# Performance work log

Hardware: AMD Instinct MI355X
Metric: run time of the kernel (lower is better)

The kernel has to match this reference:

```python
import jax, jax.numpy as jnp
import numpy as np

B, C, N = 2, 32, 4096
EPS = 1e-5


def _batchnorm1d(x, gamma, bias):
    # BatchNorm1d in training mode: stats over (batch, spatial) per channel, biased var
    mean = x.mean(axis=(0, 2), keepdims=True)
    var = x.var(axis=(0, 2), keepdims=True)
    return (x - mean) * jax.lax.rsqrt(var + EPS) * gamma[None, :, None] + bias[None, :, None]


def setup_inputs() -> dict:
    key = jax.random.key(0)
    k1, k2, k3 = jax.random.split(key, 3)
    Feature = jax.random.normal(k1, (B, C, N), dtype=jnp.float32)
    gamma = jnp.ones((C,), dtype=jnp.float32)
    bn_bias = jnp.zeros((C,), dtype=jnp.float32)
    alpha = jax.random.uniform(k2, (), dtype=jnp.float32)
    beta = jax.random.uniform(k3, (), dtype=jnp.float32)
    return {"Feature": Feature, "gamma": gamma, "bn_bias": bn_bias, "alpha": alpha, "beta": beta}


def reference(Feature, gamma, bn_bias, alpha, beta):
    a = Feature                                   # [B, C, N]
    # --- PAM: BN + ReLU prologue, then spatial N x N attention ---
    f = jax.nn.relu(_batchnorm1d(Feature, gamma, bn_bias))
    cb = jnp.einsum('bcn,bcm->bnm', f, f)         # c^T c : [B, N, N]
    s = jax.nn.softmax(cb, axis=1)                # softmax over dim=1 (as in source)
    e_p = jnp.einsum('bcn,bmn->bcm', f, s)        # c @ s^T : [B, C, N]
    pam = alpha * e_p + a
    # --- CAM: channel C x C attention, softmax over batch axis (dim=0 as in source) ---
    aa = jnp.einsum('bcn,bdn->bdc', a, a)         # matmul(a, a^T).permute(0,2,1) : [B, C, C]
    x = jax.nn.softmax(aa, axis=0)
    e_c = jnp.einsum('bji,bjn->bin', x, a)        # x^T @ a : [B, C, N]
    cam = beta * e_c + a
    return pam + cam
```

## Files before the change

### kernel.cpp

```cpp
#include <hip/hip_runtime.h>
#include <math.h>


#define BB 2
#define CC 32
#define NN 4096
#define EPSV 1e-5f

typedef short short8 __attribute__((ext_vector_type(8)));
typedef float f32x4 __attribute__((ext_vector_type(4)));

#define OFF_FNC  0
#define OFF_FCN  131072
#define OFF_M    262144
#define OFF_SC   270336
#define OFF_SH   270368
#define OFF_XW   270400
#define OFF_AAP  272448
#define OFF_Z    305216
#define OFF_EP   313408
#define ZERO_BASE 305216
#define ZERO_N4   67584

__device__ inline ushort f2bf(float x) {
    uint u = __float_as_uint(x);
    uint r = u + 0x7FFFu + ((u >> 16) & 1u);
    return (ushort)(r >> 16);
}
__device__ inline float bf2f(ushort h) { return __uint_as_float(((uint)h) << 16); }
__device__ inline uint packbf(float lo, float hi) {
    return (__float_as_uint(hi) & 0xFFFF0000u) | (__float_as_uint(lo) >> 16);
}

__global__ void __launch_bounds__(256) k_pre(const float* __restrict__ x,
                                             const float* __restrict__ gamma,
                                             const float* __restrict__ bias,
                                             float* __restrict__ ws) {
    __shared__ float smem[4352];
    const int blk = blockIdx.x, t = threadIdx.x;
    const int lane = t & 63, wv = t >> 6;
    if (blk < 32) {
        const int c = blk;
        float s = 0.f, s2 = 0.f;
        for (int i = t; i < BB * NN; i += 256) {
            const int bb = i >> 12, n = i & (NN - 1);
            const float v = x[((size_t)(bb * CC + c)) * NN + n];
            s += v; s2 += v * v;
        }
        for (int off = 32; off; off >>= 1) { s += __shfl_down(s, off); s2 += __shfl_down(s2, off); }
        if (lane == 0) { smem[wv] = s; smem[4 + wv] = s2; }
        __syncthreads();
        if (t == 0) {
            const float S = smem[0] + smem[1] + smem[2] + smem[3];
            const float S2 = smem[4] + smem[5] + smem[6] + smem[7];
            const float mean = S * (1.f / (BB * NN));
            const float var = S2 * (1.f / (BB * NN)) - mean * mean;
            const float sc = gamma[c] * rsqrtf(var + EPSV);
            ws[OFF_SC + c] = sc;
            ws[OFF_SH + c] = bias[c] - mean * sc;
        }
    } else if (blk < 96) {
        const int blk2 = blk - 32;
        const int b = blk2 >> 4, chnk = blk2 & 15;
        const int nb = chnk * 256;
        const int d = t >> 3, cg4 = (t & 7) * 4;
        float a0 = 0.f, a1 = 0.f, a2 = 0.f, a3 = 0.f;
        for (int it = 0; it < 2; ++it) {
            __syncthreads();
            for (int li = t; li < 4096; li += 256) {
                const int row = li >> 7, col = li & 127;
                smem[row * 132 + col] = x[((size_t)(b * CC + row)) * NN + nb + it * 128 + col];
            }
            __syncthreads();
            for (int k = 0; k < 128; ++k) {
                const float vd = smem[d * 132 + k];
                a0 += smem[(cg4 + 0) * 132 + k] * vd;
                a1 += smem[(cg4 + 1) * 132 + k] * vd;
                a2 += smem[(cg4 + 2) * 132 + k] * vd;
                a3 += smem[(cg4 + 3) * 132 + k] * vd;
            }
        }
        float* dst = ws + OFF_AAP + ((size_t)((b * 16 + chnk) * CC + d)) * CC + cg4;
        dst[0] = a0; dst[1] = a1; dst[2] = a2; dst[3] = a3;
    } else {
        for (int gid = (blk - 96) * 256 + t; gid < ZERO_N4; gid += 416 * 256)
            ((float4*)(ws + ZERO_BASE))[gid] = make_float4(0.f, 0.f, 0.f, 0.f);
    }
}

__global__ void __launch_bounds__(256) k_makef(const float* __restrict__ x,
                                               float* __restrict__ ws) {
    const int blk = blockIdx.x, t = threadIdx.x;
    const int ch = t & 31;
    const float sc = ws[OFF_SC + ch], sh = ws[OFF_SH + ch];
    #pragma unroll
    for (int it = 0; it < 2; ++it) {
        const int col = (t >> 5) + it * 8;
        const int idx = blk * 16 + col;
        const int b = idx >> 12, n = idx & (NN - 1);
        const float v = x[((size_t)(b * CC + ch)) * NN + n];
        const float f = fmaxf(v * sc + sh, 0.f);
        const ushort h = f2bf(f);
        const float fr = bf2f(h);
        ((ushort*)(ws + OFF_FNC))[(size_t)idx * CC + ch] = h;
        ((ushort*)(ws + OFF_FCN))[((size_t)(b * CC + ch)) * NN + n] = h;
        float s = fr * fr;
        s += __shfl_xor(s, 1); s += __shfl_xor(s, 2); s += __shfl_xor(s, 4);
        s += __shfl_xor(s, 8); s += __shfl_xor(s, 16);
        if (ch == 0) ws[OFF_M + idx] = s;
    }
    if (blk == 511) {
        for (int li = t; li < CC * CC; li += 256) {
            const int i = li >> 5, j = li & 31;
            float q0 = 0.f, q1 = 0.f;
            for (int cchunk = 0; cchunk < 16; ++cchunk) {
                q0 += ws[OFF_AAP + ((size_t)((0 * 16 + cchunk) * CC + j)) * CC + i];
                q1 += ws[OFF_AAP + ((size_t)((1 * 16 + cchunk) * CC + j)) * CC + i];
            }
            const float mx = fmaxf(q0, q1);
            const float e0 = __expf(q0 - mx), e1 = __expf(q1 - mx);
            const float inv = 1.f / (e0 + e1);
            ws[OFF_XW + 0 * 1024 + i * 32 + j] = e0 * inv;
            ws[OFF_XW + 1 * 1024 + i * 32 + j] = e1 * inv;
        }
    }
}

__global__ void __launch_bounds__(256) k_zpass(float* __restrict__ ws) {
    const ushort* fnc = (const ushort*)(ws + OFF_FNC);
    const int blk = blockIdx.x, t = threadIdx.x;
    const int lane = t & 63, wv = t >> 6;
    const int ml = lane & 15, kg = lane >> 4;
    const f32x4 fzero = {0.f, 0.f, 0.f, 0.f};
    const int b = blk >> 9;
    const int rem = blk & 511;
    const int ng = rem >> 4;
    const int mch = rem & 15;
    const int nbA = ng * 128 + wv * 16, nbB = nbA + 64;
    const short8 bfA = *(const short8*)(fnc + ((size_t)(b * NN + nbA + ml)) * CC + kg * 8);
    const short8 bfB = *(const short8*)(fnc + ((size_t)(b * NN + nbB + ml)) * CC + kg * 8);
    const float MA = ws[OFF_M + b * NN + nbA + ml];
    const float MB = ws[OFF_M + b * NN + nbB + ml];
    float zA = 0.f, zB = 0.f;
    const int m0 = mch * 256;
    for (int mm = m0; mm < m0 + 256; mm += 16) {
        const short8 af = *(const short8*)(fnc + ((size_t)(b * NN + mm + ml)) * CC + kg * 8);
        f32x4 dA = __builtin_amdgcn_mfma_f32_16x16x32_bf16(af, bfA, fzero, 0, 0, 0);
        f32x4 dB = __builtin_amdgcn_mfma_f32_16x16x32_bf16(af, bfB, fzero, 0, 0, 0);
        zA += __expf(dA[0] - MA) + __expf(dA[1] - MA) + __expf(dA[2] - MA) + __expf(dA[3] - MA);
        zB += __expf(dB[0] - MB) + __expf(dB[1] - MB) + __expf(dB[2] - MB) + __expf(dB[3] - MB);
    }
    zA += __shfl_xor(zA, 16); zA += __shfl_xor(zA, 32);
    zB += __shfl_xor(zB, 16); zB += __shfl_xor(zB, 32);
    if (lane < 16) {
        atomicAdd(ws + OFF_Z + b * NN + nbA + ml, zA);
        atomicAdd(ws + OFF_Z + b * NN + nbB + ml, zB);
    }
}

__global__ void __launch_bounds__(256) k_eppass(float* __restrict__ ws) {
    const ushort* fnc = (const ushort*)(ws + OFF_FNC);
    const ushort* fcn = (const ushort*)(ws + OFF_FCN);
    const int blk = blockIdx.x, t = threadIdx.x;
    const int lane = t & 63, wv = t >> 6;
    const int ml = lane & 15, kg = lane >> 4;
    const f32x4 fzero = {0.f, 0.f, 0.f, 0.f};
    const int b = blk >> 9;
    const int rem = blk & 511;
    const int mg = rem >> 3;
    const int nch = rem & 7;
    const int mb = mg * 64 + wv * 16;
    const short8 bm = *(const short8*)(fnc + ((size_t)(b * NN + mb + ml)) * CC + kg * 8);
    f32x4 acc0 = fzero, acc1 = fzero;
    const float* Mp = ws + OFF_M + b * NN;
    const float* Zp = ws + OFF_Z + b * NN;
    const int n0beg = nch * 512;
    for (int n0 = n0beg; n0 < n0beg + 512; n0 += 32) {
        const short8 an0 = *(const short8*)(fnc + ((size_t)(b * NN + n0      + ml)) * CC + kg * 8);
        const short8 an1 = *(const short8*)(fnc + ((size_t)(b * NN + n0 + 16 + ml)) * CC + kg * 8);
        f32x4 d0 = __builtin_amdgcn_mfma_f32_16x16x32_bf16(an0, bm, fzero, 0, 0, 0);
        f32x4 d1 = __builtin_amdgcn_mfma_f32_16x16x32_bf16(an1, bm, fzero, 0, 0, 0);
        const float4 M0 = *(const float4*)(Mp + n0 + kg * 4);
        const float4 M1 = *(const float4*)(Mp + n0 + 16 + kg * 4);
        const float4 Z0 = *(const float4*)(Zp + n0 + kg * 4);
        const float4 Z1 = *(const float4*)(Zp + n0 + 16 + kg * 4);
        const float w00 = __expf(d0[0] - M0.x) * __builtin_amdgcn_rcpf(Z0.x);
        const float w01 = __expf(d0[1] - M0.y) * __builtin_amdgcn_rcpf(Z0.y);
        const float w02 = __expf(d0[2] - M0.z) * __builtin_amdgcn_rcpf(Z0.z);
        const float w03 = __expf(d0[3] - M0.w) * __builtin_amdgcn_rcpf(Z0.w);
        const float w10 = __expf(d1[0] - M1.x) * __builtin_amdgcn_rcpf(Z1.x);
        const float w11 = __expf(d1[1] - M1.y) * __builtin_amdgcn_rcpf(Z1.y);
        const float w12 = __expf(d1[2] - M1.z) * __builtin_amdgcn_rcpf(Z1.z);
        const float w13 = __expf(d1[3] - M1.w) * __builtin_amdgcn_rcpf(Z1.w);
        const uint p0 = packbf(w00, w01), p1 = packbf(w02, w03);
        const uint q0 = packbf(w10, w11), q1 = packbf(w12, w13);
        union { uint u[4]; short8 s; } wf;
        {
            const int s0 = (((kg & 1) << 1) + 0) * 16 + ml;
            const int s1 = (((kg & 1) << 1) + 1) * 16 + ml;
            const uint vp0 = __shfl(p0, s0), vp1 = __shfl(p1, s0);
            const uint vp2 = __shfl(p0, s1), vp3 = __shfl(p1, s1);
            const uint vq0 = __shfl(q0, s0), vq1 = __shfl(q1, s0);
            const uint vq2 = __shfl(q0, s1), vq3 = __shfl(q1, s1);
            const bool hi = (kg >= 2);
            wf.u[0] = hi ? vq0 : vp0; wf.u[1] = hi ? vq1 : vp1;
            wf.u[2] = hi ? vq2 : vp2; wf.u[3] = hi ? vq3 : vp3;
        }
        const short8 a20 = *(const short8*)(fcn + ((size_t)(b * CC + ml))      * NN + n0 + kg * 8);
        const short8 a21 = *(const short8*)(fcn + ((size_t)(b * CC + 16 + ml)) * NN + n0 + kg * 8);
        acc0 = __builtin_amdgcn_mfma_f32_16x16x32_bf16(a20, wf.s, acc0, 0, 0, 0);
        acc1 = __builtin_amdgcn_mfma_f32_16x16x32_bf16(a21, wf.s, acc1, 0, 0, 0);
    }
    #pragma unroll
    for (int r = 0; r < 4; ++r) {
        atomicAdd(ws + OFF_EP + ((size_t)(b * CC + kg * 4 + r))      * NN + mb + ml, acc0[r]);
        atomicAdd(ws + OFF_EP + ((size_t)(b * CC + 16 + kg * 4 + r)) * NN + mb + ml, acc1[r]);
    }
}

__global__ void __launch_bounds__(256) k_final(const float* __restrict__ x,
                                               const float* __restrict__ alpha_p,
                                               const float* __restrict__ beta_p,
                                               const float* __restrict__ ws,
                                               float* __restrict__ out) {
    __shared__ float smem[1312];
    const int blk = blockIdx.x, t = threadIdx.x;
    const float alpha = *alpha_p, beta = *beta_p;
    float* sa = smem;
    float* sxw = smem + 256;
    const int base = blk * 16;
    const int b = base >> 12;
    for (int li = t; li < CC * CC; li += 256)
        sxw[(li >> 5) * 33 + (li & 31)] = ws[OFF_XW + b * 1024 + li];
    const int k = t >> 5, c = t & 31;
    #pragma unroll
    for (int it = 0; it < 2; ++it) {
        const int m0 = (base + it * 8) & (NN - 1);
        __syncthreads();
        { const int j = t >> 3, kc = t & 7;
          sa[j * 8 + kc] = x[((size_t)(b * CC + j)) * NN + m0 + kc]; }
        __syncthreads();
        const int m = m0 + k;
        float ec = 0.f;
        #pragma unroll
        for (int j = 0; j < CC; ++j) ec += sxw[c * 33 + j] * sa[j * 8 + k];
        const float av = sa[c * 8 + k];
        const float ep = ws[OFF_EP + ((size_t)(b * CC + c)) * NN + m];
        out[((size_t)(b * CC + c)) * NN + m] = alpha * ep + beta * ec + 2.f * av;
    }
}

extern "C" void kernel_launch(void* const* d_in, const int* in_sizes, int n_in,
                              void* d_out, int out_size, void* d_ws, size_t ws_size,
                              hipStream_t stream) {
    const float* x     = (const float*)d_in[0];
    const float* gamma = (const float*)d_in[1];
    const float* bias  = (const float*)d_in[2];
    const float* alpha = (const float*)d_in[3];
    const float* beta  = (const float*)d_in[4];
    float* out = (float*)d_out;
    float* ws  = (float*)d_ws;

    hipLaunchKernelGGL(k_pre,    dim3(512),  dim3(256), 0, stream, x, gamma, bias, ws);
    hipLaunchKernelGGL(k_makef,  dim3(512),  dim3(256), 0, stream, x, ws);
    hipLaunchKernelGGL(k_zpass,  dim3(1024), dim3(256), 0, stream, ws);
    hipLaunchKernelGGL(k_eppass, dim3(1024), dim3(256), 0, stream, ws);
    hipLaunchKernelGGL(k_final,  dim3(512),  dim3(256), 0, stream, x, alpha, beta, ws, out);
}
```

Before: 135.4 us.

## Fuse attention-weighted sum with final epilogue and restructure stats and zero passes

Merges the e_p accumulation and the final output kernel into one 512-thread block per 16 columns. Eight waves each cover a slice of N and are reduced through shared memory, which removes the global atomics and the separate EP buffer and its zero fill. BN statistics are now split across 256 blocks writing partial sums, which k_makef combines. k_makef writes one row per thread with vector stores, the CAM softmax moves into an extra zpass block, and zpass gets finer m-chunks. The cost is that k_makef runs only 32 blocks with strided 32-channel loads, and the fused kernel has fewer blocks, so parallelism drops.

```diff
diff --git a/kernel.cpp b/kernel.cpp
--- a/kernel.cpp
+++ b/kernel.cpp
@@ -13,14 +13,11 @@
 #define OFF_FNC  0
 #define OFF_FCN  131072
 #define OFF_M    262144
-#define OFF_SC   270336
-#define OFF_SH   270368
-#define OFF_XW   270400
-#define OFF_AAP  272448
-#define OFF_Z    305216
-#define OFF_EP   313408
-#define ZERO_BASE 305216
-#define ZERO_N4   67584
+#define OFF_XW   270336
+#define OFF_AAP  272384
+#define OFF_S1P  305152
+#define OFF_S2P  305408
+#define OFF_Z    305664
 
 __device__ inline ushort f2bf(float x) {
     uint u = __float_as_uint(x);
@@ -33,34 +30,26 @@
 }
 
 __global__ void __launch_bounds__(256) k_pre(const float* __restrict__ x,
-                                             const float* __restrict__ gamma,
-                                             const float* __restrict__ bias,
                                              float* __restrict__ ws) {
     __shared__ float smem[4352];
     const int blk = blockIdx.x, t = threadIdx.x;
     const int lane = t & 63, wv = t >> 6;
-    if (blk < 32) {
-        const int c = blk;
-        float s = 0.f, s2 = 0.f;
-        for (int i = t; i < BB * NN; i += 256) {
-            const int bb = i >> 12, n = i & (NN - 1);
-            const float v = x[((size_t)(bb * CC + c)) * NN + n];
-            s += v; s2 += v * v;
-        }
+    if (blk < 256) {
+        const int c = blk & 31, chunk = blk >> 5;
+        const int i0 = chunk * 1024;
+        const int b = i0 >> 12, n0 = i0 & (NN - 1);
+        const float4 v = *(const float4*)(x + ((size_t)(b * CC + c)) * NN + n0 + t * 4);
+        float s  = v.x + v.y + v.z + v.w;
+        float s2 = v.x * v.x + v.y * v.y + v.z * v.z + v.w * v.w;
         for (int off = 32; off; off >>= 1) { s += __shfl_down(s, off); s2 += __shfl_down(s2, off); }
         if (lane == 0) { smem[wv] = s; smem[4 + wv] = s2; }
         __syncthreads();
         if (t == 0) {
-            const float S = smem[0] + smem[1] + smem[2] + smem[3];
-            const float S2 = smem[4] + smem[5] + smem[6] + smem[7];
-            const float mean = S * (1.f / (BB * NN));
-            const float var = S2 * (1.f / (BB * NN)) - mean * mean;
-            const float sc = gamma[c] * rsqrtf(var + EPSV);
-            ws[OFF_SC + c] = sc;
-            ws[OFF_SH + c] = bias[c] - mean * sc;
-        }
-    } else if (blk < 96) {
-        const int blk2 = blk - 32;
+            ws[OFF_S1P + chunk * 32 + c] = smem[0] + smem[1] + smem[2] + smem[3];
+            ws[OFF_S2P + chunk * 32 + c] = smem[4] + smem[5] + smem[6] + smem[7];
+        }
+    } else {
+        const int blk2 = blk - 256;
         const int b = blk2 >> 4, chnk = blk2 & 15;
         const int nb = chnk * 256;
         const int d = t >> 3, cg4 = (t & 7) * 4;
@@ -82,34 +71,48 @@
         }
         float* dst = ws + OFF_AAP + ((size_t)((b * 16 + chnk) * CC + d)) * CC + cg4;
         dst[0] = a0; dst[1] = a1; dst[2] = a2; dst[3] = a3;
-    } else {
-        for (int gid = (blk - 96) * 256 + t; gid < ZERO_N4; gid += 416 * 256)
-            ((float4*)(ws + ZERO_BASE))[gid] = make_float4(0.f, 0.f, 0.f, 0.f);
     }
 }
 
 __global__ void __launch_bounds__(256) k_makef(const float* __restrict__ x,
+                                               const float* __restrict__ gamma,
+                                               const float* __restrict__ bias,
                                                float* __restrict__ ws) {
-    const int blk = blockIdx.x, t = threadIdx.x;
-    const int ch = t & 31;
-    const float sc = ws[OFF_SC + ch], sh = ws[OFF_SH + ch];
-    #pragma unroll
-    for (int it = 0; it < 2; ++it) {
-        const int col = (t >> 5) + it * 8;
-        const int idx = blk * 16 + col;
-        const int b = idx >> 12, n = idx & (NN - 1);
-        const float v = x[((size_t)(b * CC + ch)) * NN + n];
-        const float f = fmaxf(v * sc + sh, 0.f);
+    __shared__ float ssc[CC], ssh[CC];
+    const int blk = blockIdx.x, t = threadIdx.x;
+    if (t < CC) {
+        float S1 = 0.f, S2 = 0.f;
+        #pragma unroll
+        for (int k = 0; k < 8; ++k) { S1 += ws[OFF_S1P + k * 32 + t]; S2 += ws[OFF_S2P + k * 32 + t]; }
+        const float mean = S1 * (1.f / (BB * NN));
+        const float var = S2 * (1.f / (BB * NN)) - mean * mean;
+        const float sc = gamma[t] * rsqrtf(var + EPSV);
+        ssc[t] = sc; ssh[t] = bias[t] - mean * sc;
+    }
+    ws[OFF_Z + blk * 256 + t] = 0.f;
+    __syncthreads();
+    const int idx = blk * 256 + t;
+    const int b = idx >> 12, n = idx & (NN - 1);
+    union { ushort us[CC]; short8 v[4]; } row;
+    float msum = 0.f;
+    #pragma unroll
+    for (int c = 0; c < CC; ++c) {
+        const float v = x[((size_t)(b * CC + c)) * NN + n];
+        const float f = fmaxf(v * ssc[c] + ssh[c], 0.f);
         const ushort h = f2bf(f);
         const float fr = bf2f(h);
-        ((ushort*)(ws + OFF_FNC))[(size_t)idx * CC + ch] = h;
-        ((ushort*)(ws + OFF_FCN))[((size_t)(b * CC + ch)) * NN + n] = h;
-        float s = fr * fr;
-        s += __shfl_xor(s, 1); s += __shfl_xor(s, 2); s += __shfl_xor(s, 4);
-        s += __shfl_xor(s, 8); s += __shfl_xor(s, 16);
-        if (ch == 0) ws[OFF_M + idx] = s;
-    }
-    if (blk == 511) {
+        msum += fr * fr;
+        row.us[c] = h;
+        ((ushort*)(ws + OFF_FCN))[((size_t)(b * CC + c)) * NN + n] = h;
+    }
+    short8* dst = (short8*)((ushort*)(ws + OFF_FNC) + (size_t)idx * CC);
+    dst[0] = row.v[0]; dst[1] = row.v[1]; dst[2] = row.v[2]; dst[3] = row.v[3];
+    ws[OFF_M + idx] = msum;
+}
+
+__global__ void __launch_bounds__(256) k_zpass(float* __restrict__ ws) {
+    const int blk = blockIdx.x, t = threadIdx.x;
+    if (blk == 2048) {
         for (int li = t; li < CC * CC; li += 256) {
             const int i = li >> 5, j = li & 31;
             float q0 = 0.f, q1 = 0.f;
@@ -123,27 +126,24 @@
             ws[OFF_XW + 0 * 1024 + i * 32 + j] = e0 * inv;
             ws[OFF_XW + 1 * 1024 + i * 32 + j] = e1 * inv;
         }
-    }
-}
-
-__global__ void __launch_bounds__(256) k_zpass(float* __restrict__ ws) {
+        return;
+    }
     const ushort* fnc = (const ushort*)(ws + OFF_FNC);
-    const int blk = blockIdx.x, t = threadIdx.x;
     const int lane = t & 63, wv = t >> 6;
     const int ml = lane & 15, kg = lane >> 4;
     const f32x4 fzero = {0.f, 0.f, 0.f, 0.f};
-    const int b = blk >> 9;
-    const int rem = blk & 511;
-    const int ng = rem >> 4;
-    const int mch = rem & 15;
+    const int b = blk >> 10;
+    const int rem = blk & 1023;
+    const int ng = rem >> 5;
+    const int mch = rem & 31;
     const int nbA = ng * 128 + wv * 16, nbB = nbA + 64;
     const short8 bfA = *(const short8*)(fnc + ((size_t)(b * NN + nbA + ml)) * CC + kg * 8);
     const short8 bfB = *(const short8*)(fnc + ((size_t)(b * NN + nbB + ml)) * CC + kg * 8);
     const float MA = ws[OFF_M + b * NN + nbA + ml];
     const float MB = ws[OFF_M + b * NN + nbB + ml];
     float zA = 0.f, zB = 0.f;
-    const int m0 = mch * 256;
-    for (int mm = m0; mm < m0 + 256; mm += 16) {
+    const int m0 = mch * 128;
+    for (int mm = m0; mm < m0 + 128; mm += 16) {
         const short8 af = *(const short8*)(fnc + ((size_t)(b * NN + mm + ml)) * CC + kg * 8);
         f32x4 dA = __builtin_amdgcn_mfma_f32_16x16x32_bf16(af, bfA, fzero, 0, 0, 0);
         f32x4 dB = __builtin_amdgcn_mfma_f32_16x16x32_bf16(af, bfB, fzero, 0, 0, 0);
@@ -158,23 +158,33 @@
     }
 }
 
-__global__ void __launch_bounds__(256) k_eppass(float* __restrict__ ws) {
+__global__ void __launch_bounds__(512) k_epfinal(const float* __restrict__ x,
+                                                 const float* __restrict__ alpha_p,
+                                                 const float* __restrict__ beta_p,
+                                                 const float* __restrict__ ws,
+                                                 float* __restrict__ out) {
+    __shared__ float red[8][512];
+    __shared__ float sxw[CC * 33];
+    __shared__ float sa[CC * 16];
     const ushort* fnc = (const ushort*)(ws + OFF_FNC);
     const ushort* fcn = (const ushort*)(ws + OFF_FCN);
     const int blk = blockIdx.x, t = threadIdx.x;
     const int lane = t & 63, wv = t >> 6;
     const int ml = lane & 15, kg = lane >> 4;
     const f32x4 fzero = {0.f, 0.f, 0.f, 0.f};
-    const int b = blk >> 9;
-    const int rem = blk & 511;
-    const int mg = rem >> 3;
-    const int nch = rem & 7;
-    const int mb = mg * 64 + wv * 16;
+    const int b = blk >> 8, mg = blk & 255;
+    const int mb = mg * 16;
+
+    { const int j = t >> 4, mcol = t & 15;
+      sa[j * 16 + mcol] = x[((size_t)(b * CC + j)) * NN + mb + mcol]; }
+    for (int li = t; li < CC * CC; li += 512)
+        sxw[(li >> 5) * 33 + (li & 31)] = ws[OFF_XW + b * 1024 + li];
+
     const short8 bm = *(const short8*)(fnc + ((size_t)(b * NN + mb + ml)) * CC + kg * 8);
     f32x4 acc0 = fzero, acc1 = fzero;
     const float* Mp = ws + OFF_M + b * NN;
     const float* Zp = ws + OFF_Z + b * NN;
-    const int n0beg = nch * 512;
+    const int n0beg = wv * 512;
     for (int n0 = n0beg; n0 < n0beg + 512; n0 += 32) {
         const short8 an0 = *(const short8*)(fnc + ((size_t)(b * NN + n0      + ml)) * CC + kg * 8);
         const short8 an1 = *(const short8*)(fnc + ((size_t)(b * NN + n0 + 16 + ml)) * CC + kg * 8);
@@ -213,41 +223,20 @@
     }
     #pragma unroll
     for (int r = 0; r < 4; ++r) {
-        atomicAdd(ws + OFF_EP + ((size_t)(b * CC + kg * 4 + r))      * NN + mb + ml, acc0[r]);
-        atomicAdd(ws + OFF_EP + ((size_t)(b * CC + 16 + kg * 4 + r)) * NN + mb + ml, acc1[r]);
-    }
-}
-
-__global__ void __launch_bounds__(256) k_final(const float* __restrict__ x,
-                                               const float* __restrict__ alpha_p,
-                                               const float* __restrict__ beta_p,
-                                               const float* __restrict__ ws,
-                                               float* __restrict__ out) {
-    __shared__ float smem[1312];
-    const int blk = blockIdx.x, t = threadIdx.x;
+        red[wv][(kg * 4 + r) * 16 + ml]      = acc0[r];
+        red[wv][(16 + kg * 4 + r) * 16 + ml] = acc1[r];
+    }
+    __syncthreads();
+    float ep = 0.f;
+    #pragma unroll
+    for (int w = 0; w < 8; ++w) ep += red[w][t];
     const float alpha = *alpha_p, beta = *beta_p;
-    float* sa = smem;
-    float* sxw = smem + 256;
-    const int base = blk * 16;
-    const int b = base >> 12;
-    for (int li = t; li < CC * CC; li += 256)
-        sxw[(li >> 5) * 33 + (li & 31)] = ws[OFF_XW + b * 1024 + li];
-    const int k = t >> 5, c = t & 31;
-    #pragma unroll
-    for (int it = 0; it < 2; ++it) {
-        const int m0 = (base + it * 8) & (NN - 1);
-        __syncthreads();
-        { const int j = t >> 3, kc = t & 7;
-          sa[j * 8 + kc] = x[((size_t)(b * CC + j)) * NN + m0 + kc]; }
-        __syncthreads();
-        const int m = m0 + k;
-        float ec = 0.f;
-        #pragma unroll
-        for (int j = 0; j < CC; ++j) ec += sxw[c * 33 + j] * sa[j * 8 + k];
-        const float av = sa[c * 8 + k];
-        const float ep = ws[OFF_EP + ((size_t)(b * CC + c)) * NN + m];
-        out[((size_t)(b * CC + c)) * NN + m] = alpha * ep + beta * ec + 2.f * av;
-    }
+    const int c = t >> 4, m2 = t & 15;
+    float ec = 0.f;
+    #pragma unroll
+    for (int j = 0; j < CC; ++j) ec += sxw[c * 33 + j] * sa[j * 16 + m2];
+    const float av = sa[c * 16 + m2];
+    out[((size_t)(b * CC + c)) * NN + mb + m2] = alpha * ep + beta * ec + 2.f * av;
 }
 
 extern "C" void kernel_launch(void* const* d_in, const int* in_sizes, int n_in,
@@ -261,9 +250,8 @@
     float* out = (float*)d_out;
     float* ws  = (float*)d_ws;
 
-    hipLaunchKernelGGL(k_pre,    dim3(512),  dim3(256), 0, stream, x, gamma, bias, ws);
-    hipLaunchKernelGGL(k_makef,  dim3(512),  dim3(256), 0, stream, x, ws);
-    hipLaunchKernelGGL(k_zpass,  dim3(1024), dim3(256), 0, stream, ws);
-    hipLaunchKernelGGL(k_eppass, dim3(1024), dim3(256), 0, stream, ws);
-    hipLaunchKernelGGL(k_final,  dim3(512),  dim3(256), 0, stream, x, alpha, beta, ws, out);
-}
+    hipLaunchKernelGGL(k_pre,     dim3(288),  dim3(256), 0, stream, x, ws);
+    hipLaunchKernelGGL(k_makef,   dim3(32),   dim3(256), 0, stream, x, gamma, bias, ws);
+    hipLaunchKernelGGL(k_zpass,   dim3(2049), dim3(256), 0, stream, ws);
+    hipLaunchKernelGGL(k_epfinal, dim3(512),  dim3(512), 0, stream, x, alpha, beta, ws, out);
+}
```

After: 129.1 us. 4.7% less time.
